# Performance work log

Hardware: AMD Instinct MI355X
Metric: run time of the kernel (lower is better)

The kernel has to match this reference:

```python
import jax, jax.numpy as jnp
import numpy as np
import math

B, T, C, H = 8, 512, 768, 12
ADJ_F = 12  # adj feature dim (adj_proj1 in_features)


def setup_inputs() -> dict:
    key = jax.random.key(0)
    ks = jax.random.split(key, 16)
    s = 0.02
    x = jax.random.normal(ks[0], (B, T, C), jnp.float32)
    # 1.0 marks a padded position; keep first token valid in every row
    pad = (jax.random.uniform(ks[1], (B, T)) > 0.8).astype(jnp.float32)
    pad = pad.at[:, 0].set(0.0)
    adj = jax.random.normal(ks[2], (B, T, T, ADJ_F), jnp.float32)
    # torch Linear convention: W is [out, in]
    Wq = jax.random.normal(ks[3], (C, C), jnp.float32) * s
    bq = jnp.zeros((C,), jnp.float32)
    Wk = jax.random.normal(ks[4], (C, C), jnp.float32) * s
    bk = jnp.zeros((C,), jnp.float32)
    Wv = jax.random.normal(ks[5], (C, C), jnp.float32) * s
    bv = jnp.zeros((C,), jnp.float32)
    Wp = jax.random.normal(ks[6], (C, C), jnp.float32) * s
    bp = jnp.zeros((C,), jnp.float32)
    A1 = jax.random.normal(ks[7], (2 * H, ADJ_F), jnp.float32) * s  # adj_proj1, no bias
    A2 = jax.random.normal(ks[8], (H, 2 * H), jnp.float32) * s     # adj_proj2, no bias
    adj_weight = jnp.float32(50.0)
    return dict(x=x, x_padding_judge=pad, adj=adj, Wq=Wq, bq=bq, Wk=Wk, bk=bk,
                Wv=Wv, bv=bv, Wp=Wp, bp=bp, A1=A1, A2=A2, adj_weight=adj_weight)


def reference(x, x_padding_judge, adj, Wq, bq, Wk, bk, Wv, bv, Wp, bp, A1, A2, adj_weight):
    Bx, Tx, Cx = x.shape
    hd = Cx // H
    # pairwise validity mask: [B,T,T]
    keep = 1.0 - x_padding_judge
    mask = keep[:, :, None] * keep[:, None, :]
    split = lambda h: h.reshape(Bx, Tx, H, hd).transpose(0, 2, 1, 3)  # [B,H,T,hd]
    q = split(x @ Wq.T + bq)
    k = split(x @ Wk.T + bk)
    v = split(x @ Wv.T + bv)
    att = jnp.einsum('bhqd,bhkd->bhqk', q, k) * (1.0 / math.sqrt(hd))
    # eval mode: attn_drop is identity, so the dropout-of-ones trick leaves mask unchanged
    att = jnp.where(mask[:, None, :, :] == 0.0, jnp.float32(-1e9), att)
    att = jax.nn.softmax(att, axis=-1)
    # adjacency-derived bias added AFTER softmax
    att_fix = jax.nn.gelu(jnp.einsum('bqkf,ef->bqke', adj, A1), approximate=False)
    att_fix = jnp.einsum('bqke,he->bqkh', att_fix, A2).transpose(0, 3, 1, 2)  # [B,H,T,T]
    att = att + adj_weight * att_fix
    y = jnp.einsum('bhqk,bhkd->bhqd', att, v)
    y = y.transpose(0, 2, 1, 3).reshape(Bx, Tx, Cx)
    return y @ Wp.T + bp  # resid_drop is identity in eval
```

## Files before the change

### kernel.cpp

```cpp
#include <hip/hip_runtime.h>
#include <math.h>

#define TT 512
#define CC 768
#define NH 12
#define HD 64
#define ADJF 12

typedef __attribute__((ext_vector_type(8))) short bf16x8;
typedef __attribute__((ext_vector_type(4))) short bf16x4;
typedef __attribute__((ext_vector_type(4))) float f32x4;
typedef __attribute__((ext_vector_type(2))) float f32x2v;
typedef __attribute__((ext_vector_type(2))) __bf16 bf16x2v;

__device__ __forceinline__ ushort f2bf(float x) {
    union { __bf16 b; ushort u; } c; c.b = (__bf16)x; return c.u;
}
__device__ __forceinline__ unsigned f2bf2(float lo, float hi) {
    f32x2v s; s[0] = lo; s[1] = hi;
    union { bf16x2v b; unsigned u; } c;
    c.b = __builtin_convertvector(s, bf16x2v);
    return c.u;
}

#define MFMA16(a, b, c) __builtin_amdgcn_mfma_f32_16x16x32_bf16((a), (b), (c), 0, 0, 0)

__device__ __forceinline__ f32x4 MFMA16K(bf16x4 a, bf16x4 b, f32x4 c) {
#if __has_builtin(__builtin_amdgcn_mfma_f32_16x16x16bf16_1k)
    return __builtin_amdgcn_mfma_f32_16x16x16bf16_1k(a, b, c, 0, 0, 0);
#else
    f32x4 d;
    asm("v_mfma_f32_16x16x16_bf16 %0, %1, %2, %3"
        : "=v"(d) : "v"(a), "v"(b), "v"(c));
    return d;
#endif
}

__global__ __launch_bounds__(256)
void cast5(const float* __restrict__ x,  const float* __restrict__ wq,
           const float* __restrict__ wk, const float* __restrict__ wv,
           const float* __restrict__ wp,
           ushort* __restrict__ xb,  ushort* __restrict__ wqb,
           ushort* __restrict__ wkb, ushort* __restrict__ wvb,
           ushort* __restrict__ wpb)
{
    const float* src; ushort* dst; int n8;
    switch (blockIdx.y) {
      case 0:  src = x;  dst = xb;  n8 = 393216; break;
      case 1:  src = wq; dst = wqb; n8 = 73728;  break;
      case 2:  src = wk; dst = wkb; n8 = 73728;  break;
      case 3:  src = wv; dst = wvb; n8 = 73728;  break;
      default: src = wp; dst = wpb; n8 = 73728;  break;
    }
    int i = blockIdx.x * 256 + threadIdx.x;
    if (i >= n8) return;
    float4 a = ((const float4*)src)[2 * i];
    float4 b = ((const float4*)src)[2 * i + 1];
    uint4 o;
    o.x = f2bf2(a.x, a.y);
    o.y = f2bf2(a.z, a.w);
    o.z = f2bf2(b.x, b.y);
    o.w = f2bf2(b.z, b.w);
    ((uint4*)dst)[i] = o;
}

__device__ __forceinline__ void mfma_gemm_acc(
    const ushort* __restrict__ A, const ushort* __restrict__ B,
    f32x4 (&acc)[4][4], ushort* As, ushort* Bs)
{
    const int t = threadIdx.x;
    const int bm = blockIdx.x, bn = blockIdx.y;
    const int w = t >> 6, lane = t & 63, lx = lane & 15, quad = lane >> 4;
    const int wr = w >> 1, wc = w & 1;
    const int sr = t >> 1, sh = (t & 1) << 4;

    const ushort* Arow = A + (size_t)(bm * 128 + sr) * CC + sh;
    const ushort* Brow = B + (size_t)(bn * 128 + sr) * CC + sh;

    uint4 a0 = *(const uint4*)(Arow);
    uint4 a1 = *(const uint4*)(Arow + 8);
    uint4 b0 = *(const uint4*)(Brow);
    uint4 b1 = *(const uint4*)(Brow + 8);
    *(uint4*)&As[sr * 40 + sh]     = a0;
    *(uint4*)&As[sr * 40 + sh + 8] = a1;
    *(uint4*)&Bs[sr * 40 + sh]     = b0;
    *(uint4*)&Bs[sr * 40 + sh + 8] = b1;

    for (int kb = 0; kb < 24; kb++) {
        __syncthreads();
        const int cur = (kb & 1) * 5120, nxt = ((kb + 1) & 1) * 5120;
        if (kb < 23) {
            a0 = *(const uint4*)(Arow + (kb + 1) * 32);
            a1 = *(const uint4*)(Arow + (kb + 1) * 32 + 8);
            b0 = *(const uint4*)(Brow + (kb + 1) * 32);
            b1 = *(const uint4*)(Brow + (kb + 1) * 32 + 8);
        }
        bf16x8 af[4], bfr[4];
#pragma unroll
        for (int mt = 0; mt < 4; mt++)
            af[mt] = *(const bf16x8*)&As[cur + (wr * 64 + mt * 16 + lx) * 40 + quad * 8];
#pragma unroll
        for (int nt = 0; nt < 4; nt++)
            bfr[nt] = *(const bf16x8*)&Bs[cur + (wc * 64 + nt * 16 + lx) * 40 + quad * 8];
#pragma unroll
        for (int mt = 0; mt < 4; mt++)
#pragma unroll
            for (int nt = 0; nt < 4; nt++)
                acc[mt][nt] = MFMA16(af[mt], bfr[nt], acc[mt][nt]);
        if (kb < 23) {
            *(uint4*)&As[nxt + sr * 40 + sh]     = a0;
            *(uint4*)&As[nxt + sr * 40 + sh + 8] = a1;
            *(uint4*)&Bs[nxt + sr * 40 + sh]     = b0;
            *(uint4*)&Bs[nxt + sr * 40 + sh + 8] = b1;
        }
    }
}

__global__ __launch_bounds__(256)
void qkv_mfma(const ushort* __restrict__ xb,
              const ushort* __restrict__ Wqb, const float* __restrict__ bq,
              const ushort* __restrict__ Wkb, const float* __restrict__ bk,
              const ushort* __restrict__ Wvb, const float* __restrict__ bv,
              ushort* __restrict__ Qb, ushort* __restrict__ Kb,
              ushort* __restrict__ VtB)
{
    __shared__ ushort As[10240], Bs[10240];
    const int z = blockIdx.z;
    const ushort* W   = (z == 0) ? Wqb : (z == 1) ? Wkb : Wvb;
    const float* bias = (z == 0) ? bq  : (z == 1) ? bk  : bv;

    f32x4 acc[4][4];
#pragma unroll
    for (int i = 0; i < 4; i++)
#pragma unroll
        for (int j = 0; j < 4; j++) acc[i][j] = (f32x4){0.f, 0.f, 0.f, 0.f};

    mfma_gemm_acc(xb, W, acc, As, Bs);

    const int t = threadIdx.x;
    const int w = t >> 6, lane = t & 63, lx = lane & 15, quad = lane >> 4;
    const int wr = w >> 1, wc = w & 1;
    const int bm = blockIdx.x, bn = blockIdx.y;

    float bvv[4];
#pragma unroll
    for (int nt = 0; nt < 4; nt++)
        bvv[nt] = bias[bn * 128 + wc * 64 + nt * 16 + lx];

    if (z < 2) {
        ushort* O = (z == 0) ? Qb : Kb;
#pragma unroll
        for (int mt = 0; mt < 4; mt++) {
            int m0 = bm * 128 + wr * 64 + mt * 16 + quad * 4;
            int bb = m0 >> 9, q = m0 & 511;
#pragma unroll
            for (int nt = 0; nt < 4; nt++) {
                int n = bn * 128 + wc * 64 + nt * 16 + lx;
                int hh = n >> 6, d = n & 63;
                size_t base = ((size_t)(bb * NH + hh) * TT + q) * HD + d;
#pragma unroll
                for (int i = 0; i < 4; i++)
                    O[base + (size_t)i * HD] = f2bf(acc[mt][nt][i] + bvv[nt]);
            }
        }
    } else {
#pragma unroll
        for (int mt = 0; mt < 4; mt++) {
            int m0 = bm * 128 + wr * 64 + mt * 16 + quad * 4;
            int bb = m0 >> 9, k = m0 & 511;
            int kt = k >> 6, kw = k & 63;
#pragma unroll
            for (int nt = 0; nt < 4; nt++) {
                int n = bn * 128 + wc * 64 + nt * 16 + lx;
                int hh = n >> 6, d = n & 63;
                uint2 pk;
                pk.x = f2bf2(acc[mt][nt][0] + bvv[nt], acc[mt][nt][1] + bvv[nt]);
                pk.y = f2bf2(acc[mt][nt][2] + bvv[nt], acc[mt][nt][3] + bvv[nt]);
                *(uint2*)&VtB[(size_t)((bb * NH + hh) * 8 + kt) * 4096 + d * 64 + kw] = pk;
            }
        }
    }
}

__global__ __launch_bounds__(256)
void proj_mfma(const ushort* __restrict__ y1, const ushort* __restrict__ Wpb,
               const float* __restrict__ bp, float* __restrict__ out)
{
    __shared__ ushort As[10240], Bs[10240];
    f32x4 acc[4][4];
#pragma unroll
    for (int i = 0; i < 4; i++)
#pragma unroll
        for (int j = 0; j < 4; j++) acc[i][j] = (f32x4){0.f, 0.f, 0.f, 0.f};

    mfma_gemm_acc(y1, Wpb, acc, As, Bs);

    const int t = threadIdx.x;
    const int w = t >> 6, lane = t & 63, lx = lane & 15, quad = lane >> 4;
    const int wr = w >> 1, wc = w & 1;
    const int bm = blockIdx.x, bn = blockIdx.y;
#pragma unroll
    for (int nt = 0; nt < 4; nt++) {
        int n = bn * 128 + wc * 64 + nt * 16 + lx;
        float bvv = bp[n];
#pragma unroll
        for (int mt = 0; mt < 4; mt++) {
            int m0 = bm * 128 + wr * 64 + mt * 16 + quad * 4;
#pragma unroll
            for (int i = 0; i < 4; i++)
                out[(size_t)(m0 + i) * CC + n] = acc[mt][nt][i] + bvv;
        }
    }
}

__device__ __forceinline__ float gelu_s(float x) {
    float x2 = x * x;
    float u  = __builtin_fmaf(x2, 0.025f, -0.166666666666667f);
    u        = __builtin_fmaf(x2, u, 1.0f);
    float er = 0.79788456080286536f * x * u;
    return 0.5f * x * (1.0f + er);
}

__global__ __launch_bounds__(256)
void adj_f_mfma(const float* __restrict__ adj, const float* __restrict__ A1,
                const float* __restrict__ A2, const float* __restrict__ adjw_p,
                ushort* __restrict__ Fb)
{
    __shared__ float A1s[288];
    __shared__ float A2s[288];

    const int t = threadIdx.x;
    for (int i = t; i < 288; i += 256) { A1s[i] = A1[i]; A2s[i] = A2[i]; }
    __syncthreads();

    const int w = t >> 6, lane = t & 63, lx = lane & 15, qd = lane >> 4;
    const int q = blockIdx.x, b = blockIdx.y;
    const float adjw = adjw_p[0];

    union { bf16x8 v; ushort u[8]; } b1a, b1b;
#pragma unroll
    for (int j = 0; j < 8; j++) {
        int f = qd * 8 + j;
        b1a.u[j] = (f < 12) ? f2bf(A1s[lx * 12 + f]) : (ushort)0;
        b1b.u[j] = (lx < 8 && f < 12) ? f2bf(A1s[(16 + lx) * 12 + f]) : (ushort)0;
    }
    union { bf16x4 v; ushort u[4]; } B2lo, B2hi;
#pragma unroll
    for (int j = 0; j < 4; j++) {
        int elo = qd * 4 + j;
        int ehi = 16 + qd * 4 + j;
        B2lo.u[j] = (lx < 12) ? f2bf(adjw * A2s[lx * 24 + elo]) : (ushort)0;
        B2hi.u[j] = (lx < 12 && ehi < 24) ? f2bf(adjw * A2s[lx * 24 + ehi]) : (ushort)0;
    }

    const size_t prow = ((size_t)b * TT + q) * TT;
    ushort* outq = Fb + ((size_t)(b * NH) * TT + q) * TT;

    const float* arow = adj + (prow + w * 16 + lx) * ADJF;

    float4 c0 = (float4){0.f, 0.f, 0.f, 0.f}, c1 = c0;
    if (qd == 0)      { c0 = *(const float4*)(arow); c1 = *(const float4*)(arow + 4); }
    else if (qd == 1) { c0 = *(const float4*)(arow + 8); }

    for (int it = 0; it < 8; it++) {
        const int k0 = it * 64 + w * 16;

        const float* nrow = arow + 64 * ADJF;
        float4 n0 = c0, n1 = c1;
        if (it < 7) {
            if (qd == 0)      { n0 = *(const float4*)(nrow); n1 = *(const float4*)(nrow + 4); }
            else if (qd == 1) { n0 = *(const float4*)(nrow + 8); }
        }
        arow = nrow;

        union { bf16x8 v; unsigned u[4]; } afr;
        afr.u[0] = f2bf2(c0.x, c0.y);
        afr.u[1] = f2bf2(c0.z, c0.w);
        if (qd == 0) { afr.u[2] = f2bf2(c1.x, c1.y); afr.u[3] = f2bf2(c1.z, c1.w); }
        else         { afr.u[2] = 0;                 afr.u[3] = 0; }

        f32x4 zz = (f32x4){0.f, 0.f, 0.f, 0.f};
        f32x4 c1a = MFMA16(b1a.v, afr.v, zz);
        f32x4 c1b = MFMA16(b1b.v, afr.v, zz);

        union { bf16x4 v; unsigned u[2]; } ga, gb;
        ga.u[0] = f2bf2(gelu_s(c1a[0]), gelu_s(c1a[1]));
        ga.u[1] = f2bf2(gelu_s(c1a[2]), gelu_s(c1a[3]));
        gb.u[0] = f2bf2(gelu_s(c1b[0]), gelu_s(c1b[1]));
        gb.u[1] = f2bf2(gelu_s(c1b[2]), gelu_s(c1b[3]));

        f32x4 c2 = MFMA16K(ga.v, B2lo.v, MFMA16K(gb.v, B2hi.v, zz));

        if (lx < 12) {
            uint2 pk;
            pk.x = f2bf2(c2[0], c2[1]);
            pk.y = f2bf2(c2[2], c2[3]);
            *(uint2*)&outq[(size_t)lx * TT * TT + k0 + qd * 4] = pk;
        }

        c0 = n0; c1 = n1;
    }
}

__global__ __launch_bounds__(256)
void flash_mfma(const ushort* __restrict__ Qh, const ushort* __restrict__ Kh,
                const ushort* __restrict__ VtB, const ushort* __restrict__ Fb,
                const float* __restrict__ pad, ushort* __restrict__ y1)
{
    __shared__ ushort Ps[4][16][72];

    const int t = threadIdx.x, w = t >> 6, lane = t & 63;
    const int lx = lane & 15, quad = lane >> 4;

    const int id  = blockIdx.x + 8 * blockIdx.y + 96 * blockIdx.z;
    const int xcd = id & 7, j = id >> 3;
    const int pair = xcd * 12 + (j >> 3);
    const int qt  = j & 7;
    const int h   = pair % NH, b = pair / NH;

    const int q0 = qt * 64;
    const int bh = b * NH + h;

    const ushort* Qrow = Qh + ((size_t)bh * TT + q0 + w * 16 + lx) * HD + quad * 8;
    bf16x8 qa0 = *(const bf16x8*)Qrow;
    bf16x8 qa1 = *(const bf16x8*)(Qrow + 32);

    const float kq = 1.0f - pad[b * TT + q0 + w * 16 + lx];

    f32x4 o[4], o2[4];
#pragma unroll
    for (int i = 0; i < 4; i++) {
        o[i]  = (f32x4){0.f, 0.f, 0.f, 0.f};
        o2[i] = (f32x4){0.f, 0.f, 0.f, 0.f};
    }
    float ls = 0.f;

    const ushort* Frow  = Fb + (size_t)(bh * TT + q0 + w * 16 + lx) * TT + quad * 8;
    const float*  padk  = pad + b * TT;
    const ushort* Vbase = VtB + (size_t)bh * 8 * 4096;

    for (int ck = 0; ck < 8; ck++) {
        const int k0 = ck * 64;

        bf16x8 ka[4][2];
        float4 kp[4];
#pragma unroll
        for (int mt = 0; mt < 4; mt++) {
            const ushort* Krow = Kh + ((size_t)bh * TT + k0 + mt * 16 + lx) * HD + quad * 8;
            ka[mt][0] = *(const bf16x8*)Krow;
            ka[mt][1] = *(const bf16x8*)(Krow + 32);
            kp[mt] = *(const float4*)&padk[k0 + mt * 16 + quad * 4];
        }
        bf16x8 vb[4][2];
#pragma unroll
        for (int nt = 0; nt < 4; nt++) {
            const ushort* Vrow = Vbase + (size_t)ck * 4096 + (nt * 16 + lx) * 64 + quad * 8;
            vb[nt][0] = *(const bf16x8*)Vrow;
            vb[nt][1] = *(const bf16x8*)(Vrow + 32);
        }
        bf16x8 fa0 = *(const bf16x8*)(Frow + k0);
        bf16x8 fa1 = *(const bf16x8*)(Frow + k0 + 32);

        f32x4 st[4];
#pragma unroll
        for (int mt = 0; mt < 4; mt++) {
            f32x4 z = (f32x4){0.f, 0.f, 0.f, 0.f};
            z = MFMA16(ka[mt][0], qa0, z);
            z = MFMA16(ka[mt][1], qa1, z);
            st[mt] = z;
        }

#pragma unroll
        for (int mt = 0; mt < 4; mt++) {
            float pv[4];
#pragma unroll
            for (int i = 0; i < 4; i++) {
                float kpad = ((const float*)&kp[mt])[i];
                float p = __builtin_amdgcn_exp2f(st[mt][i] * 0.18033688011112042f);
                p = (kpad != 0.0f) ? 0.0f : p;
                p = (kq == 0.0f) ? 1.0f : p;
                pv[i] = p; ls += p;
            }
            uint2 pk;
            pk.x = f2bf2(pv[0], pv[1]);
            pk.y = f2bf2(pv[2], pv[3]);
            *(uint2*)&Ps[w][lx][mt * 16 + quad * 4] = pk;
        }
        asm volatile("s_waitcnt lgkmcnt(0)" ::: "memory");
        bf16x8 pa0 = *(const bf16x8*)&Ps[w][lx][quad * 8];
        bf16x8 pa1 = *(const bf16x8*)&Ps[w][lx][32 + quad * 8];

#pragma unroll
        for (int nt = 0; nt < 4; nt++) {
            o[nt]  = MFMA16(pa0, vb[nt][0], o[nt]);
            o[nt]  = MFMA16(pa1, vb[nt][1], o[nt]);
            o2[nt] = MFMA16(fa0, vb[nt][0], o2[nt]);
            o2[nt] = MFMA16(fa1, vb[nt][1], o2[nt]);
        }
    }
    ls += __shfl_xor(ls, 16, 64);
    ls += __shfl_xor(ls, 32, 64);
    float inv[4];
#pragma unroll
    for (int i = 0; i < 4; i++)
        inv[i] = 1.0f / __shfl(ls, quad * 4 + i, 16);
#pragma unroll
    for (int nt = 0; nt < 4; nt++)
#pragma unroll
        for (int i = 0; i < 4; i++)
            y1[(size_t)(b * TT + q0 + w * 16 + quad * 4 + i) * CC + h * HD + nt * 16 + lx] =
                f2bf(o[nt][i] * inv[i] + o2[nt][i]);
}

extern "C" void kernel_launch(void* const* d_in, const int* in_sizes, int n_in,
                              void* d_out, int out_size, void* d_ws, size_t ws_size,
                              hipStream_t stream)
{
    const float* x    = (const float*)d_in[0];
    const float* pad  = (const float*)d_in[1];
    const float* adj  = (const float*)d_in[2];
    const float* Wq   = (const float*)d_in[3];
    const float* bq   = (const float*)d_in[4];
    const float* Wk   = (const float*)d_in[5];
    const float* bk   = (const float*)d_in[6];
    const float* Wv   = (const float*)d_in[7];
    const float* bv   = (const float*)d_in[8];
    const float* Wp   = (const float*)d_in[9];
    const float* bp   = (const float*)d_in[10];
    const float* A1   = (const float*)d_in[11];
    const float* A2   = (const float*)d_in[12];
    const float* adjw = (const float*)d_in[13];

    ushort* ws  = (ushort*)d_ws;
    ushort* Fb  = ws;
    ushort* Qb  = Fb + 25165824;
    ushort* Kb  = Qb + 3145728;
    ushort* Vt  = Kb + 3145728;
    ushort* y1  = Vt + 3145728;
    ushort* xb  = y1 + 3145728;
    ushort* Wqb = xb + 3145728;
    ushort* Wkb = Wqb + 589824;
    ushort* Wvb = Wkb + 589824;
    ushort* Wpb = Wvb + 589824;
    float*  out = (float*)d_out;

    cast5<<<dim3(1536, 5), 256, 0, stream>>>(x, Wq, Wk, Wv, Wp,
                                             xb, Wqb, Wkb, Wvb, Wpb);
    qkv_mfma<<<dim3(32, 6, 3), 256, 0, stream>>>(xb, Wqb, bq, Wkb, bk, Wvb, bv,
                                                 Qb, Kb, Vt);
    adj_f_mfma<<<dim3(512, 8), 256, 0, stream>>>(adj, A1, A2, adjw, Fb);
    flash_mfma<<<dim3(8, 12, 8), 256, 0, stream>>>(Qb, Kb, Vt, Fb, pad, y1);
    proj_mfma<<<dim3(32, 6), 256, 0, stream>>>(y1, Wpb, bp, out);
}
```

Measured before the change: 303.0 us.

## Split adjacency transform across cast and QKV kernels to overlap work

Removes the standalone adjacency-feature kernel and interleaves its blocks into the cast kernel (first half of query rows) and the QKV GEMM kernel (second half) via a flat block index decoded into roles. This lets the memory-bound adjacency pass run concurrently with the cast and the MFMA GEMM, filling idle CUs and removing one launch. The adj blocks in the QKV kernel inherit the 40KB shared allocation, which may lower occupancy for them.

```diff
diff --git a/kernel.cpp b/kernel.cpp
--- a/kernel.cpp
+++ b/kernel.cpp
@@ -36,23 +36,176 @@
 #endif
 }
 
+__device__ __forceinline__ float gelu_s(float x) {
+    float x2 = x * x;
+    float u  = __builtin_fmaf(x2, 0.025f, -0.166666666666667f);
+    u        = __builtin_fmaf(x2, u, 1.0f);
+    float er = 0.79788456080286536f * x * u;
+    return 0.5f * x * (1.0f + er);
+}
+
+__device__ __forceinline__ void adj_body(
+    const float* __restrict__ adj, const float* __restrict__ A1,
+    const float* __restrict__ A2, const float* __restrict__ adjw_p,
+    ushort* __restrict__ Fb, float* A1s, float* A2s, int q, int b)
+{
+    const int t = threadIdx.x;
+    for (int i = t; i < 288; i += 256) { A1s[i] = A1[i]; A2s[i] = A2[i]; }
+    __syncthreads();
+
+    const int w = t >> 6, lane = t & 63, lx = lane & 15, qd = lane >> 4;
+    const float adjw = adjw_p[0];
+
+    union { bf16x8 v; ushort u[8]; } b1a, b1b;
+#pragma unroll
+    for (int j = 0; j < 8; j++) {
+        int f = qd * 8 + j;
+        b1a.u[j] = (f < 12) ? f2bf(A1s[lx * 12 + f]) : (ushort)0;
+        b1b.u[j] = (lx < 8 && f < 12) ? f2bf(A1s[(16 + lx) * 12 + f]) : (ushort)0;
+    }
+    union { bf16x4 v; ushort u[4]; } B2lo, B2hi;
+#pragma unroll
+    for (int j = 0; j < 4; j++) {
+        int elo = qd * 4 + j;
+        int ehi = 16 + qd * 4 + j;
+        B2lo.u[j] = (lx < 12) ? f2bf(adjw * A2s[lx * 24 + elo]) : (ushort)0;
+        B2hi.u[j] = (lx < 12 && ehi < 24) ? f2bf(adjw * A2s[lx * 24 + ehi]) : (ushort)0;
+    }
+
+    const size_t prow = ((size_t)b * TT + q) * TT;
+    ushort* outq = Fb + ((size_t)(b * NH) * TT + q) * TT;
+
+    const float* arow = adj + (prow + w * 16 + lx) * ADJF;
+
+    float4 c0 = (float4){0.f, 0.f, 0.f, 0.f}, c1 = c0;
+    if (qd == 0)      { c0 = *(const float4*)(arow); c1 = *(const float4*)(arow + 4); }
+    else if (qd == 1) { c0 = *(const float4*)(arow + 8); }
+
+    for (int it = 0; it < 8; it++) {
+        const int k0 = it * 64 + w * 16;
+
+        const float* nrow = arow + 64 * ADJF;
+        float4 n0 = c0, n1 = c1;
+        if (it < 7) {
+            if (qd == 0)      { n0 = *(const float4*)(nrow); n1 = *(const float4*)(nrow + 4); }
+            else if (qd == 1) { n0 = *(const float4*)(nrow + 8); }
+        }
+        arow = nrow;
+
+        union { bf16x8 v; unsigned u[4]; } afr;
+        afr.u[0] = f2bf2(c0.x, c0.y);
+        afr.u[1] = f2bf2(c0.z, c0.w);
+        if (qd == 0) { afr.u[2] = f2bf2(c1.x, c1.y); afr.u[3] = f2bf2(c1.z, c1.w); }
+        else         { afr.u[2] = 0;                 afr.u[3] = 0; }
+
+        f32x4 zz = (f32x4){0.f, 0.f, 0.f, 0.f};
+        f32x4 c1a = MFMA16(b1a.v, afr.v, zz);
+        f32x4 c1b = MFMA16(b1b.v, afr.v, zz);
+
+        union { bf16x4 v; unsigned u[2]; } ga, gb;
+        ga.u[0] = f2bf2(gelu_s(c1a[0]), gelu_s(c1a[1]));
+        ga.u[1] = f2bf2(gelu_s(c1a[2]), gelu_s(c1a[3]));
+        gb.u[0] = f2bf2(gelu_s(c1b[0]), gelu_s(c1b[1]));
+        gb.u[1] = f2bf2(gelu_s(c1b[2]), gelu_s(c1b[3]));
+
+        f32x4 c2 = MFMA16K(ga.v, B2lo.v, MFMA16K(gb.v, B2hi.v, zz));
+
+        if (lx < 12) {
+            uint2 pk;
+            pk.x = f2bf2(c2[0], c2[1]);
+            pk.y = f2bf2(c2[2], c2[3]);
+            *(uint2*)&outq[(size_t)lx * TT * TT + k0 + qd * 4] = pk;
+        }
+
+        c0 = n0; c1 = n1;
+    }
+}
+
+__device__ __forceinline__ void mfma_gemm_acc(
+    const ushort* __restrict__ A, const ushort* __restrict__ B,
+    f32x4 (&acc)[4][4], ushort* As, ushort* Bs, int bm, int bn)
+{
+    const int t = threadIdx.x;
+    const int w = t >> 6, lane = t & 63, lx = lane & 15, quad = lane >> 4;
+    const int wr = w >> 1, wc = w & 1;
+    const int sr = t >> 1, sh = (t & 1) << 4;
+
+    const ushort* Arow = A + (size_t)(bm * 128 + sr) * CC + sh;
+    const ushort* Brow = B + (size_t)(bn * 128 + sr) * CC + sh;
+
+    uint4 a0 = *(const uint4*)(Arow);
+    uint4 a1 = *(const uint4*)(Arow + 8);
+    uint4 b0 = *(const uint4*)(Brow);
+    uint4 b1 = *(const uint4*)(Brow + 8);
+    *(uint4*)&As[sr * 40 + sh]     = a0;
+    *(uint4*)&As[sr * 40 + sh + 8] = a1;
+    *(uint4*)&Bs[sr * 40 + sh]     = b0;
+    *(uint4*)&Bs[sr * 40 + sh + 8] = b1;
+
+    for (int kb = 0; kb < 24; kb++) {
+        __syncthreads();
+        const int cur = (kb & 1) * 5120, nxt = ((kb + 1) & 1) * 5120;
+        if (kb < 23) {
+            a0 = *(const uint4*)(Arow + (kb + 1) * 32);
+            a1 = *(const uint4*)(Arow + (kb + 1) * 32 + 8);
+            b0 = *(const uint4*)(Brow + (kb + 1) * 32);
+            b1 = *(const uint4*)(Brow + (kb + 1) * 32 + 8);
+        }
+        bf16x8 af[4], bfr[4];
+#pragma unroll
+        for (int mt = 0; mt < 4; mt++)
+            af[mt] = *(const bf16x8*)&As[cur + (wr * 64 + mt * 16 + lx) * 40 + quad * 8];
+#pragma unroll
+        for (int nt = 0; nt < 4; nt++)
+            bfr[nt] = *(const bf16x8*)&Bs[cur + (wc * 64 + nt * 16 + lx) * 40 + quad * 8];
+#pragma unroll
+        for (int mt = 0; mt < 4; mt++)
+#pragma unroll
+            for (int nt = 0; nt < 4; nt++)
+                acc[mt][nt] = MFMA16(af[mt], bfr[nt], acc[mt][nt]);
+        if (kb < 23) {
+            *(uint4*)&As[nxt + sr * 40 + sh]     = a0;
+            *(uint4*)&As[nxt + sr * 40 + sh + 8] = a1;
+            *(uint4*)&Bs[nxt + sr * 40 + sh]     = b0;
+            *(uint4*)&Bs[nxt + sr * 40 + sh + 8] = b1;
+        }
+    }
+}
+
 __global__ __launch_bounds__(256)
-void cast5(const float* __restrict__ x,  const float* __restrict__ wq,
-           const float* __restrict__ wk, const float* __restrict__ wv,
-           const float* __restrict__ wp,
-           ushort* __restrict__ xb,  ushort* __restrict__ wqb,
-           ushort* __restrict__ wkb, ushort* __restrict__ wvb,
-           ushort* __restrict__ wpb)
-{
+void cast_adj(const float* __restrict__ x,  const float* __restrict__ wq,
+              const float* __restrict__ wk, const float* __restrict__ wv,
+              const float* __restrict__ wp,
+              ushort* __restrict__ xb,  ushort* __restrict__ wqb,
+              ushort* __restrict__ wkb, ushort* __restrict__ wvb,
+              ushort* __restrict__ wpb,
+              const float* __restrict__ adj, const float* __restrict__ A1,
+              const float* __restrict__ A2, const float* __restrict__ adjw_p,
+              ushort* __restrict__ Fb)
+{
+    __shared__ float A1s[288];
+    __shared__ float A2s[288];
+
+    const int bid = blockIdx.x;
+    const int g = bid / 19, r = bid % 19;
+
+    if (r < 4) {
+        const int idx = g * 4 + r;
+        adj_body(adj, A1, A2, adjw_p, Fb, A1s, A2s, idx & 255, idx >> 8);
+        return;
+    }
+
+    const int cidx = g * 15 + (r - 4);
+    const int bx = cidx % 1536, by = cidx / 1536;
     const float* src; ushort* dst; int n8;
-    switch (blockIdx.y) {
+    switch (by) {
       case 0:  src = x;  dst = xb;  n8 = 393216; break;
       case 1:  src = wq; dst = wqb; n8 = 73728;  break;
       case 2:  src = wk; dst = wkb; n8 = 73728;  break;
       case 3:  src = wv; dst = wvb; n8 = 73728;  break;
       default: src = wp; dst = wpb; n8 = 73728;  break;
     }
-    int i = blockIdx.x * 256 + threadIdx.x;
+    int i = bx * 256 + threadIdx.x;
     if (i >= n8) return;
     float4 a = ((const float4*)src)[2 * i];
     float4 b = ((const float4*)src)[2 * i + 1];
@@ -64,68 +217,34 @@
     ((uint4*)dst)[i] = o;
 }
 
-__device__ __forceinline__ void mfma_gemm_acc(
-    const ushort* __restrict__ A, const ushort* __restrict__ B,
-    f32x4 (&acc)[4][4], ushort* As, ushort* Bs)
-{
-    const int t = threadIdx.x;
-    const int bm = blockIdx.x, bn = blockIdx.y;
-    const int w = t >> 6, lane = t & 63, lx = lane & 15, quad = lane >> 4;
-    const int wr = w >> 1, wc = w & 1;
-    const int sr = t >> 1, sh = (t & 1) << 4;
-
-    const ushort* Arow = A + (size_t)(bm * 128 + sr) * CC + sh;
-    const ushort* Brow = B + (size_t)(bn * 128 + sr) * CC + sh;
-
-    uint4 a0 = *(const uint4*)(Arow);
-    uint4 a1 = *(const uint4*)(Arow + 8);
-    uint4 b0 = *(const uint4*)(Brow);
-    uint4 b1 = *(const uint4*)(Brow + 8);
-    *(uint4*)&As[sr * 40 + sh]     = a0;
-    *(uint4*)&As[sr * 40 + sh + 8] = a1;
-    *(uint4*)&Bs[sr * 40 + sh]     = b0;
-    *(uint4*)&Bs[sr * 40 + sh + 8] = b1;
-
-    for (int kb = 0; kb < 24; kb++) {
-        __syncthreads();
-        const int cur = (kb & 1) * 5120, nxt = ((kb + 1) & 1) * 5120;
-        if (kb < 23) {
-            a0 = *(const uint4*)(Arow + (kb + 1) * 32);
-            a1 = *(const uint4*)(Arow + (kb + 1) * 32 + 8);
-            b0 = *(const uint4*)(Brow + (kb + 1) * 32);
-            b1 = *(const uint4*)(Brow + (kb + 1) * 32 + 8);
-        }
-        bf16x8 af[4], bfr[4];
-#pragma unroll
-        for (int mt = 0; mt < 4; mt++)
-            af[mt] = *(const bf16x8*)&As[cur + (wr * 64 + mt * 16 + lx) * 40 + quad * 8];
-#pragma unroll
-        for (int nt = 0; nt < 4; nt++)
-            bfr[nt] = *(const bf16x8*)&Bs[cur + (wc * 64 + nt * 16 + lx) * 40 + quad * 8];
-#pragma unroll
-        for (int mt = 0; mt < 4; mt++)
-#pragma unroll
-            for (int nt = 0; nt < 4; nt++)
-                acc[mt][nt] = MFMA16(af[mt], bfr[nt], acc[mt][nt]);
-        if (kb < 23) {
-            *(uint4*)&As[nxt + sr * 40 + sh]     = a0;
-            *(uint4*)&As[nxt + sr * 40 + sh + 8] = a1;
-            *(uint4*)&Bs[nxt + sr * 40 + sh]     = b0;
-            *(uint4*)&Bs[nxt + sr * 40 + sh + 8] = b1;
-        }
-    }
-}
-
 __global__ __launch_bounds__(256)
-void qkv_mfma(const ushort* __restrict__ xb,
-              const ushort* __restrict__ Wqb, const float* __restrict__ bq,
-              const ushort* __restrict__ Wkb, const float* __restrict__ bk,
-              const ushort* __restrict__ Wvb, const float* __restrict__ bv,
-              ushort* __restrict__ Qb, ushort* __restrict__ Kb,
-              ushort* __restrict__ VtB)
-{
-    __shared__ ushort As[10240], Bs[10240];
-    const int z = blockIdx.z;
+void qkv_adj(const ushort* __restrict__ xb,
+             const ushort* __restrict__ Wqb, const float* __restrict__ bq,
+             const ushort* __restrict__ Wkb, const float* __restrict__ bk,
+             const ushort* __restrict__ Wvb, const float* __restrict__ bv,
+             ushort* __restrict__ Qb, ushort* __restrict__ Kb,
+             ushort* __restrict__ VtB,
+             const float* __restrict__ adj, const float* __restrict__ A1,
+             const float* __restrict__ A2, const float* __restrict__ adjw_p,
+             ushort* __restrict__ Fb)
+{
+    __shared__ __align__(16) ushort sh[20480];
+
+    const int bid = blockIdx.x;
+    const int g = bid / 41, r = bid % 41;
+
+    if (r >= 9) {
+        const int idx = g * 32 + (r - 9);
+        adj_body(adj, A1, A2, adjw_p, Fb,
+                 (float*)sh, (float*)(sh + 576), 256 + (idx & 255), idx >> 8);
+        return;
+    }
+
+    const int qidx = g * 9 + r;
+    const int bm = qidx % 32, bn = (qidx / 32) % 6, z = qidx / 192;
+
+    ushort* As = sh;
+    ushort* Bs = sh + 10240;
     const ushort* W   = (z == 0) ? Wqb : (z == 1) ? Wkb : Wvb;
     const float* bias = (z == 0) ? bq  : (z == 1) ? bk  : bv;
 
@@ -135,12 +254,11 @@
 #pragma unroll
         for (int j = 0; j < 4; j++) acc[i][j] = (f32x4){0.f, 0.f, 0.f, 0.f};
 
-    mfma_gemm_acc(xb, W, acc, As, Bs);
+    mfma_gemm_acc(xb, W, acc, As, Bs, bm, bn);
 
     const int t = threadIdx.x;
     const int w = t >> 6, lane = t & 63, lx = lane & 15, quad = lane >> 4;
     const int wr = w >> 1, wc = w & 1;
-    const int bm = blockIdx.x, bn = blockIdx.y;
 
     float bvv[4];
 #pragma unroll
@@ -193,7 +311,7 @@
 #pragma unroll
         for (int j = 0; j < 4; j++) acc[i][j] = (f32x4){0.f, 0.f, 0.f, 0.f};
 
-    mfma_gemm_acc(y1, Wpb, acc, As, Bs);
+    mfma_gemm_acc(y1, Wpb, acc, As, Bs, blockIdx.x, blockIdx.y);
 
     const int t = threadIdx.x;
     const int w = t >> 6, lane = t & 63, lx = lane & 15, quad = lane >> 4;
@@ -210,95 +328,6 @@
             for (int i = 0; i < 4; i++)
                 out[(size_t)(m0 + i) * CC + n] = acc[mt][nt][i] + bvv;
         }
-    }
-}
-
-__device__ __forceinline__ float gelu_s(float x) {
-    float x2 = x * x;
-    float u  = __builtin_fmaf(x2, 0.025f, -0.166666666666667f);
-    u        = __builtin_fmaf(x2, u, 1.0f);
-    float er = 0.79788456080286536f * x * u;
-    return 0.5f * x * (1.0f + er);
-}
-
-__global__ __launch_bounds__(256)
-void adj_f_mfma(const float* __restrict__ adj, const float* __restrict__ A1,
-                const float* __restrict__ A2, const float* __restrict__ adjw_p,
-                ushort* __restrict__ Fb)
-{
-    __shared__ float A1s[288];
-    __shared__ float A2s[288];
-
-    const int t = threadIdx.x;
-    for (int i = t; i < 288; i += 256) { A1s[i] = A1[i]; A2s[i] = A2[i]; }
-    __syncthreads();
-
-    const int w = t >> 6, lane = t & 63, lx = lane & 15, qd = lane >> 4;
-    const int q = blockIdx.x, b = blockIdx.y;
-    const float adjw = adjw_p[0];
-
-    union { bf16x8 v; ushort u[8]; } b1a, b1b;
-#pragma unroll
-    for (int j = 0; j < 8; j++) {
-        int f = qd * 8 + j;
-        b1a.u[j] = (f < 12) ? f2bf(A1s[lx * 12 + f]) : (ushort)0;
-        b1b.u[j] = (lx < 8 && f < 12) ? f2bf(A1s[(16 + lx) * 12 + f]) : (ushort)0;
-    }
-    union { bf16x4 v; ushort u[4]; } B2lo, B2hi;
-#pragma unroll
-    for (int j = 0; j < 4; j++) {
-        int elo = qd * 4 + j;
-        int ehi = 16 + qd * 4 + j;
-        B2lo.u[j] = (lx < 12) ? f2bf(adjw * A2s[lx * 24 + elo]) : (ushort)0;
-        B2hi.u[j] = (lx < 12 && ehi < 24) ? f2bf(adjw * A2s[lx * 24 + ehi]) : (ushort)0;
-    }
-
-    const size_t prow = ((size_t)b * TT + q) * TT;
-    ushort* outq = Fb + ((size_t)(b * NH) * TT + q) * TT;
-
-    const float* arow = adj + (prow + w * 16 + lx) * ADJF;
-
-    float4 c0 = (float4){0.f, 0.f, 0.f, 0.f}, c1 = c0;
-    if (qd == 0)      { c0 = *(const float4*)(arow); c1 = *(const float4*)(arow + 4); }
-    else if (qd == 1) { c0 = *(const float4*)(arow + 8); }
-
-    for (int it = 0; it < 8; it++) {
-        const int k0 = it * 64 + w * 16;
-
-        const float* nrow = arow + 64 * ADJF;
-        float4 n0 = c0, n1 = c1;
-        if (it < 7) {
-            if (qd == 0)      { n0 = *(const float4*)(nrow); n1 = *(const float4*)(nrow + 4); }
-            else if (qd == 1) { n0 = *(const float4*)(nrow + 8); }
-        }
-        arow = nrow;
-
-        union { bf16x8 v; unsigned u[4]; } afr;
-        afr.u[0] = f2bf2(c0.x, c0.y);
-        afr.u[1] = f2bf2(c0.z, c0.w);
-        if (qd == 0) { afr.u[2] = f2bf2(c1.x, c1.y); afr.u[3] = f2bf2(c1.z, c1.w); }
-        else         { afr.u[2] = 0;                 afr.u[3] = 0; }
-
-        f32x4 zz = (f32x4){0.f, 0.f, 0.f, 0.f};
-        f32x4 c1a = MFMA16(b1a.v, afr.v, zz);
-        f32x4 c1b = MFMA16(b1b.v, afr.v, zz);
-
-        union { bf16x4 v; unsigned u[2]; } ga, gb;
-        ga.u[0] = f2bf2(gelu_s(c1a[0]), gelu_s(c1a[1]));
-        ga.u[1] = f2bf2(gelu_s(c1a[2]), gelu_s(c1a[3]));
-        gb.u[0] = f2bf2(gelu_s(c1b[0]), gelu_s(c1b[1]));
-        gb.u[1] = f2bf2(gelu_s(c1b[2]), gelu_s(c1b[3]));
-
-        f32x4 c2 = MFMA16K(ga.v, B2lo.v, MFMA16K(gb.v, B2hi.v, zz));
-
-        if (lx < 12) {
-            uint2 pk;
-            pk.x = f2bf2(c2[0], c2[1]);
-            pk.y = f2bf2(c2[2], c2[3]);
-            *(uint2*)&outq[(size_t)lx * TT * TT + k0 + qd * 4] = pk;
-        }
-
-        c0 = n0; c1 = n1;
     }
 }
 
@@ -444,11 +473,12 @@
     ushort* Wpb = Wvb + 589824;
     float*  out = (float*)d_out;
 
-    cast5<<<dim3(1536, 5), 256, 0, stream>>>(x, Wq, Wk, Wv, Wp,
-                                             xb, Wqb, Wkb, Wvb, Wpb);
-    qkv_mfma<<<dim3(32, 6, 3), 256, 0, stream>>>(xb, Wqb, bq, Wkb, bk, Wvb, bv,
-                                                 Qb, Kb, Vt);
-    adj_f_mfma<<<dim3(512, 8), 256, 0, stream>>>(adj, A1, A2, adjw, Fb);
+    cast_adj<<<9728, 256, 0, stream>>>(x, Wq, Wk, Wv, Wp,
+                                       xb, Wqb, Wkb, Wvb, Wpb,
+                                       adj, A1, A2, adjw, Fb);
+    qkv_adj<<<2624, 256, 0, stream>>>(xb, Wqb, bq, Wkb, bk, Wvb, bv,
+                                      Qb, Kb, Vt,
+                                      adj, A1, A2, adjw, Fb);
     flash_mfma<<<dim3(8, 12, 8), 256, 0, stream>>>(Qb, Kb, Vt, Fb, pad, y1);
     proj_mfma<<<dim3(32, 6), 256, 0, stream>>>(y1, Wpb, bp, out);
 }
```

Result: slower. 322.6 us (+6.4%).

## Stage adj rows via async global-to-LDS loads and coalesce F writes through LDS

Applied to the files above, without the earlier changes.

The adj projection kernel now streams each wave's adj rows into double-buffered LDS with global_load_lds, replacing the strided per-lane float4 register loads. Its bf16 output tile for all 12 heads is collected in shared memory and written back as fully coalesced 4-byte rows after a block barrier, replacing the scattered 8-byte stores. The aim is to improve global load and store coalescing on this bandwidth-bound kernel. The cost is more LDS use, which may lower occupancy, plus an extra block-wide barrier and a full vmcnt wait each iteration.

```diff
diff --git a/kernel.cpp b/kernel.cpp
--- a/kernel.cpp
+++ b/kernel.cpp
@@ -228,6 +228,8 @@
 {
     __shared__ float A1s[288];
     __shared__ float A2s[288];
+    __shared__ __align__(16) float adjS[4][2][192];
+    __shared__ __align__(8)  ushort Fs[12 * 516];
 
     const int t = threadIdx.x;
     for (int i = t; i < 288; i += 256) { A1s[i] = A1[i]; A2s[i] = A2[i]; }
@@ -254,30 +256,49 @@
     }
 
     const size_t prow = ((size_t)b * TT + q) * TT;
-    ushort* outq = Fb + ((size_t)(b * NH) * TT + q) * TT;
-
-    const float* arow = adj + (prow + w * 16 + lx) * ADJF;
-
-    float4 c0 = (float4){0.f, 0.f, 0.f, 0.f}, c1 = c0;
-    if (qd == 0)      { c0 = *(const float4*)(arow); c1 = *(const float4*)(arow + 4); }
-    else if (qd == 1) { c0 = *(const float4*)(arow + 8); }
+
+#if __has_builtin(__builtin_amdgcn_global_load_lds)
+    const char* gbase = (const char*)(adj + (prow + w * 16) * ADJF);
+#pragma unroll
+    for (int c = 0; c < 3; c++)
+        __builtin_amdgcn_global_load_lds(
+            (const __attribute__((address_space(1))) void*)(gbase + c * 256 + lane * 4),
+            (__attribute__((address_space(3))) void*)&adjS[w][0][c * 64], 4, 0, 0);
+#endif
 
     for (int it = 0; it < 8; it++) {
         const int k0 = it * 64 + w * 16;
-
-        const float* nrow = arow + 64 * ADJF;
-        float4 n0 = c0, n1 = c1;
+        const int buf = it & 1;
+
+#if __has_builtin(__builtin_amdgcn_global_load_lds)
+        asm volatile("s_waitcnt vmcnt(0)" ::: "memory");
+        __builtin_amdgcn_sched_barrier(0);
         if (it < 7) {
-            if (qd == 0)      { n0 = *(const float4*)(nrow); n1 = *(const float4*)(nrow + 4); }
-            else if (qd == 1) { n0 = *(const float4*)(nrow + 8); }
-        }
-        arow = nrow;
+            const char* gn = gbase + (size_t)(it + 1) * 3072;
+#pragma unroll
+            for (int c = 0; c < 3; c++)
+                __builtin_amdgcn_global_load_lds(
+                    (const __attribute__((address_space(1))) void*)(gn + c * 256 + lane * 4),
+                    (__attribute__((address_space(3))) void*)&adjS[w][buf ^ 1][c * 64], 4, 0, 0);
+        }
+        const float* L = &adjS[w][buf][lx * 12];
+#else
+        const float* L = adj + (prow + k0 + lx) * ADJF;
+#endif
 
         union { bf16x8 v; unsigned u[4]; } afr;
-        afr.u[0] = f2bf2(c0.x, c0.y);
-        afr.u[1] = f2bf2(c0.z, c0.w);
-        if (qd == 0) { afr.u[2] = f2bf2(c1.x, c1.y); afr.u[3] = f2bf2(c1.z, c1.w); }
-        else         { afr.u[2] = 0;                 afr.u[3] = 0; }
+        if (qd == 0) {
+            float4 u0 = *(const float4*)(L);
+            float4 u1 = *(const float4*)(L + 4);
+            afr.u[0] = f2bf2(u0.x, u0.y); afr.u[1] = f2bf2(u0.z, u0.w);
+            afr.u[2] = f2bf2(u1.x, u1.y); afr.u[3] = f2bf2(u1.z, u1.w);
+        } else if (qd == 1) {
+            float4 u0 = *(const float4*)(L + 8);
+            afr.u[0] = f2bf2(u0.x, u0.y); afr.u[1] = f2bf2(u0.z, u0.w);
+            afr.u[2] = 0; afr.u[3] = 0;
+        } else {
+            afr.u[0] = 0; afr.u[1] = 0; afr.u[2] = 0; afr.u[3] = 0;
+        }
 
         f32x4 zz = (f32x4){0.f, 0.f, 0.f, 0.f};
         f32x4 c1a = MFMA16(b1a.v, afr.v, zz);
@@ -295,10 +316,16 @@
             uint2 pk;
             pk.x = f2bf2(c2[0], c2[1]);
             pk.y = f2bf2(c2[2], c2[3]);
-            *(uint2*)&outq[(size_t)lx * TT * TT + k0 + qd * 4] = pk;
-        }
-
-        c0 = n0; c1 = n1;
+            *(uint2*)&Fs[lx * 516 + k0 + qd * 4] = pk;
+        }
+    }
+
+    __syncthreads();
+    ushort* outb = Fb + (size_t)b * NH * TT * TT + (size_t)q * TT;
+#pragma unroll
+    for (int h = 0; h < NH; h++) {
+        unsigned v = *(const unsigned*)&Fs[h * 516 + t * 2];
+        *(unsigned*)&outb[(size_t)h * TT * TT + t * 2] = v;
     }
 }
 
```

New measurement: 301.2 us. Within noise of the previous version (-0.6%).
